# Performance work log

Hardware: AMD Instinct MI355X
Metric: run time of the kernel (lower is better)

Reference implementation:

```python
import jax, jax.numpy as jnp
import numpy as np

INF = 1e20


def setup_inputs() -> dict:
    key = jax.random.key(0)
    k1, k2, k3 = jax.random.split(key, 3)
    B, Q, M, F, D = 16, 64, 512, 16, 512
    return {
        "query_embed": jax.random.normal(k1, (B, Q, D), dtype=jnp.float32),
        "in_memory_embed": jax.random.normal(k2, (B, M, F, D), dtype=jnp.float32),
        "out_memory_embed": jax.random.normal(k3, (B, M, F, D), dtype=jnp.float32),
        "ctx_mask": jnp.ones((B, M, F), dtype=jnp.float32),
        "query_mask": jnp.ones((B, Q), dtype=jnp.float32),
    }


def reference(query_embed, in_memory_embed, out_memory_embed, ctx_mask, query_mask):
    # co-attention scores: [B, Q, M, F]
    attention = jnp.einsum("bqd,bmfd->bqmf", query_embed, in_memory_embed)
    # additive INF masking (torch: mask*att - (1-mask)*INF)
    cm = ctx_mask[:, None, :, :]            # [B,1,M,F]
    attention = cm * attention - (1.0 - cm) * INF
    qm = query_mask[:, :, None, None]       # [B,Q,1,1]
    attention = qm * attention - (1.0 - qm) * INF
    # NOTE: torch code computes a max-pool over Q for kb_feature_att but
    # immediately overwrites it with softmax of a ones/ctx mask -> dead code.
    mask = ctx_mask * 1.0 - (1.0 - ctx_mask) * INF        # [B,M,F]
    kb_feature_att = jax.nn.softmax(mask, axis=-1)        # [B,M,F]
    # weighted read over feature slots: [B,M,D]
    in_mem = jnp.einsum("bmf,bmfd->bmd", kb_feature_att, in_memory_embed)
    out_mem = out_memory_embed.sum(axis=2)                # [B,M,D]
    # max-pool over feature axis F -> [B,Q,M]
    att_qm = attention.max(axis=-1)
    probs = jax.nn.softmax(att_qm, axis=-1)               # over M
    new_query_embed = query_embed + jnp.einsum("bqm,bmd->bqd", probs, out_mem)
    probs2 = jax.nn.softmax(att_qm, axis=1)               # over Q
    in_mem = in_mem + jnp.einsum("bqm,bqd->bmd", probs2, new_query_embed)
    return (new_query_embed, in_mem, out_mem)
```

## Files before the change

kernel.cpp:

```cpp
#include <hip/hip_runtime.h>

#define INF_F 1e20f
#define B_ 16
#define Q_ 64
#define M_ 512
#define F_ 16
#define D_ 512

typedef __attribute__((ext_vector_type(8))) short short8v;
typedef __attribute__((ext_vector_type(4))) float f32x4;

static __device__ __forceinline__ float bits_f(unsigned int u) { return __uint_as_float(u); }

static __device__ __forceinline__ int lds_off(int row, int gran) {
    return row * 40 + ((gran ^ (row & 3)) << 3);
}

static __device__ __forceinline__ void split4(float4 v, uint2& H, uint2& L) {
    unsigned hx = __float_as_uint(v.x) & 0xffff0000u, hy = __float_as_uint(v.y) & 0xffff0000u;
    unsigned hz = __float_as_uint(v.z) & 0xffff0000u, hw = __float_as_uint(v.w) & 0xffff0000u;
    H.x = (hx >> 16) | hy;
    H.y = (hz >> 16) | hw;
    L.x = (__float_as_uint(v.x - bits_f(hx)) >> 16) | (__float_as_uint(v.y - bits_f(hy)) & 0xffff0000u);
    L.y = (__float_as_uint(v.z - bits_f(hz)) >> 16) | (__float_as_uint(v.w - bits_f(hw)) & 0xffff0000u);
}

static __device__ __forceinline__ void conv_store(short* __restrict__ Hb, short* __restrict__ Lb,
                                                  int row, int c, float4 v) {
    uint2 H, L;
    split4(v, H, L);
    int off = row * 40 + (((c >> 1) ^ (row & 3)) << 3) + ((c & 1) << 2);
    *(uint2*)&Hb[off] = H;
    *(uint2*)&Lb[off] = L;
}

__global__ __launch_bounds__(256) void k_q_split(
    const float* __restrict__ q, uint2* __restrict__ qh, uint2* __restrict__ ql)
{
    int fid = blockIdx.x * 256 + threadIdx.x;
    float4 v = ((const float4*)q)[fid];
    int col = fid & 127, row = (fid >> 7) & 63, b = fid >> 13;
    int kc = col >> 3, sub = col & 7;
    uint2 H, L;
    split4(v, H, L);
    size_t oidx = ((size_t)(b * 16 + kc) * 512) + row * 8 + sub;
    qh[oidx] = H;
    ql[oidx] = L;
}

__global__ __launch_bounds__(256) void k_att_mfma(
    const uint2* __restrict__ qhg, const uint2* __restrict__ qlg,
    const float* __restrict__ in_mem, const float* __restrict__ out_mem,
    const float* __restrict__ ctx_mask, const float* __restrict__ query_mask,
    float* __restrict__ att_qm, float* __restrict__ in_mem_base,
    float* __restrict__ out_mem_sum)
{
    __shared__ __align__(16) short Qh[2][2560];
    __shared__ __align__(16) short Ql[2][2560];
    __shared__ __align__(16) short Mh[2][2560];
    __shared__ __align__(16) short Ml[2][2560];

    const int bid = blockIdx.x;
    const int b   = bid & 15;
    const int m0  = (bid >> 4) * 4;
    const int t   = threadIdx.x;
    const int w   = t >> 6;
    const int lane = t & 63;
    const int lr  = lane & 15;
    const int lg  = lane >> 4;
    const int r0  = (t >> 3) * 2, r1 = r0 + 1;
    const int scol = t & 7;
    const int f0  = r0 & 15, f1 = f0 + 1;

    float w0, w1;
    {
        const float* cm = ctx_mask + ((size_t)b * M_ + m0 + w) * F_;
        float wv[F_]; float mx = -INF_F;
        #pragma unroll
        for (int f = 0; f < F_; ++f) {
            float cv = cm[f];
            float v = cv - (1.0f - cv) * INF_F;
            wv[f] = v; mx = fmaxf(mx, v);
        }
        float s = 0.f;
        #pragma unroll
        for (int f = 0; f < F_; ++f) { wv[f] = __expf(wv[f] - mx); s += wv[f]; }
        float inv = 1.0f / s;
        w0 = wv[f0] * inv; w1 = wv[f1] * inv;
    }

    const float4* m4 = (const float4*)in_mem;
    const float4* o4 = (const float4*)out_mem;
    const size_t mbase = ((size_t)b * M_ + m0) * F_ * 128;
    const size_t qimg  = (size_t)b * 16 * 512;

    f32x4 acc[4];
    #pragma unroll
    for (int j = 0; j < 4; ++j) acc[j] = (f32x4){0, 0, 0, 0};

    uint2 qhA[2], qlA[2], qhB[2], qlB[2];
    float4 mA[2], oA[2], mB[2], oB[2];

#define LOAD_CHUNK(qh_, ql_, m_, o_, kc) do { int k4 = (kc) * 8;               \
        qh_[0] = qhg[qimg + (size_t)(kc) * 512 + t];                           \
        qh_[1] = qhg[qimg + (size_t)(kc) * 512 + t + 256];                     \
        ql_[0] = qlg[qimg + (size_t)(kc) * 512 + t];                           \
        ql_[1] = qlg[qimg + (size_t)(kc) * 512 + t + 256];                     \
        m_[0] = m4[mbase + (size_t)r0 * 128 + k4 + scol];                      \
        m_[1] = m4[mbase + (size_t)r1 * 128 + k4 + scol];                      \
        o_[0] = o4[mbase + (size_t)r0 * 128 + k4 + scol];                      \
        o_[1] = o4[mbase + (size_t)r1 * 128 + k4 + scol]; } while (0)

#define CONV(qh_, ql_, m_, bi) do {                                            \
        _Pragma("unroll")                                                      \
        for (int i = 0; i < 2; ++i) {                                          \
            int idx = t + i * 256, row = idx >> 3, sub = idx & 7;              \
            int off = row * 40 + (((sub >> 1) ^ (row & 3)) << 3) + ((sub & 1) << 2); \
            *(uint2*)&Qh[bi][off] = qh_[i];                                    \
            *(uint2*)&Ql[bi][off] = ql_[i];                                    \
        }                                                                      \
        conv_store(Mh[bi], Ml[bi], r0, scol, m_[0]);                           \
        conv_store(Mh[bi], Ml[bi], r1, scol, m_[1]); } while (0)

#define BARRIER() do { asm volatile("s_waitcnt lgkmcnt(0)" ::: "memory");      \
        __builtin_amdgcn_s_barrier(); } while (0)

#define MFMA_RED(bi, m_, o_, kc) do {                                          \
        short8v bh = *(const short8v*)&Mh[bi][lds_off(w * 16 + lr, lg)];       \
        short8v bl = *(const short8v*)&Ml[bi][lds_off(w * 16 + lr, lg)];       \
        _Pragma("unroll")                                                      \
        for (int tq = 0; tq < 4; ++tq) {                                       \
            short8v ah = *(const short8v*)&Qh[bi][lds_off(tq * 16 + lr, lg)];  \
            short8v al = *(const short8v*)&Ql[bi][lds_off(tq * 16 + lr, lg)];  \
            acc[tq] = __builtin_amdgcn_mfma_f32_16x16x32_bf16(ah, bh, acc[tq], 0, 0, 0); \
            acc[tq] = __builtin_amdgcn_mfma_f32_16x16x32_bf16(ah, bl, acc[tq], 0, 0, 0); \
            acc[tq] = __builtin_amdgcn_mfma_f32_16x16x32_bf16(al, bh, acc[tq], 0, 0, 0); \
        }                                                                      \
        float4 pin, pout;                                                      \
        pin.x = w0 * m_[0].x + w1 * m_[1].x;  pin.y = w0 * m_[0].y + w1 * m_[1].y; \
        pin.z = w0 * m_[0].z + w1 * m_[1].z;  pin.w = w0 * m_[0].w + w1 * m_[1].w; \
        pout.x = o_[0].x + o_[1].x;  pout.y = o_[0].y + o_[1].y;               \
        pout.z = o_[0].z + o_[1].z;  pout.w = o_[0].w + o_[1].w;               \
        _Pragma("unroll")                                                      \
        for (int sh = 8; sh <= 32; sh <<= 1) {                                 \
            pin.x += __shfl_xor(pin.x, sh, 64);  pin.y += __shfl_xor(pin.y, sh, 64);  \
            pin.z += __shfl_xor(pin.z, sh, 64);  pin.w += __shfl_xor(pin.w, sh, 64);  \
            pout.x += __shfl_xor(pout.x, sh, 64); pout.y += __shfl_xor(pout.y, sh, 64); \
            pout.z += __shfl_xor(pout.z, sh, 64); pout.w += __shfl_xor(pout.w, sh, 64); \
        }                                                                      \
        if (lane < 8) {                                                        \
            size_t oi = ((size_t)b * M_ + m0 + w) * 128 + (kc) * 8 + lane;     \
            ((float4*)in_mem_base)[oi] = pin;                                  \
            ((float4*)out_mem_sum)[oi] = pout;                                 \
        } } while (0)

    LOAD_CHUNK(qhA, qlA, mA, oA, 0);
    #pragma unroll
    for (int it = 0; it < 8; ++it) {
        int kc0 = 2 * it, kc1 = 2 * it + 1;
        LOAD_CHUNK(qhB, qlB, mB, oB, kc1);
        CONV(qhA, qlA, mA, 0);
        BARRIER();
        MFMA_RED(0, mA, oA, kc0);
        if (it < 7) LOAD_CHUNK(qhA, qlA, mA, oA, kc0 + 2);
        CONV(qhB, qlB, mB, 1);
        BARRIER();
        MFMA_RED(1, mB, oB, kc1);
    }

    {
        int m = m0 + w;
        float cmv = ctx_mask[((size_t)b * M_ + m) * F_ + lr];
        #pragma unroll
        for (int tq = 0; tq < 4; ++tq) {
            #pragma unroll
            for (int rg = 0; rg < 4; ++rg) {
                int q = tq * 16 + lg * 4 + rg;
                float qmv = query_mask[b * Q_ + q];
                float v = acc[tq][rg];
                v = cmv * v - (1.0f - cmv) * INF_F;
                v = qmv * v - (1.0f - qmv) * INF_F;
                #pragma unroll
                for (int sh = 1; sh < 16; sh <<= 1) v = fmaxf(v, __shfl_xor(v, sh, 64));
                if (lr == 0)
                    att_qm[((size_t)b * Q_ + q) * M_ + m] = v;
            }
        }
    }
#undef LOAD_CHUNK
#undef CONV
#undef BARRIER
#undef MFMA_RED
}

__global__ __launch_bounds__(128) void k_new_query(
    const float* __restrict__ att, const float* __restrict__ query,
    const float* __restrict__ out_sum, float* __restrict__ new_q)
{
    __shared__ float P[8][512];
    int bid = blockIdx.x;
    int b = bid & 15, qc = bid >> 4;
    int t = threadIdx.x;
    {
        int qi = t >> 4, l16 = t & 15;
        const float* row = att + ((size_t)b * Q_ + qc * 8 + qi) * M_;
        float vals[32]; float mx = -INF_F;
        #pragma unroll
        for (int i = 0; i < 32; ++i) { vals[i] = row[l16 + i * 16]; mx = fmaxf(mx, vals[i]); }
        #pragma unroll
        for (int s = 1; s < 16; s <<= 1) mx = fmaxf(mx, __shfl_xor(mx, s, 64));
        float sm = 0.f;
        #pragma unroll
        for (int i = 0; i < 32; ++i) { vals[i] = __expf(vals[i] - mx); sm += vals[i]; }
        #pragma unroll
        for (int s = 1; s < 16; s <<= 1) sm += __shfl_xor(sm, s, 64);
        float inv = 1.0f / sm;
        #pragma unroll
        for (int i = 0; i < 32; ++i) P[qi][l16 + i * 16] = vals[i] * inv;
    }
    __syncthreads();
    int c = t;
    const float4* o4 = (const float4*)out_sum + (size_t)b * M_ * 128 + c;
    const float4* q4 = (const float4*)query + ((size_t)b * Q_ + qc * 8) * 128 + c;
    float4 acc[8];
    #pragma unroll
    for (int qi = 0; qi < 8; ++qi) acc[qi] = q4[(size_t)qi * 128];
    for (int mm = 0; mm < M_; mm += 4) {
        float4 o0 = o4[(size_t)(mm + 0) * 128];
        float4 o1 = o4[(size_t)(mm + 1) * 128];
        float4 o2 = o4[(size_t)(mm + 2) * 128];
        float4 o3 = o4[(size_t)(mm + 3) * 128];
        #pragma unroll
        for (int qi = 0; qi < 8; ++qi) {
            float4 p = *(const float4*)&P[qi][mm];
            acc[qi].x += p.x * o0.x + p.y * o1.x + p.z * o2.x + p.w * o3.x;
            acc[qi].y += p.x * o0.y + p.y * o1.y + p.z * o2.y + p.w * o3.y;
            acc[qi].z += p.x * o0.z + p.y * o1.z + p.z * o2.z + p.w * o3.z;
            acc[qi].w += p.x * o0.w + p.y * o1.w + p.z * o2.w + p.w * o3.w;
        }
    }
    float4* n4 = (float4*)new_q + ((size_t)b * Q_ + qc * 8) * 128 + c;
    #pragma unroll
    for (int qi = 0; qi < 8; ++qi) n4[(size_t)qi * 128] = acc[qi];
}

__global__ __launch_bounds__(128) void k_in_mem(
    const float* __restrict__ att, const float* __restrict__ new_q,
    float* __restrict__ in_mem_io)
{
    __shared__ float P[8][64];
    int bid = blockIdx.x;
    int b = bid & 15, mc = bid >> 4;
    int m0 = mc * 8;
    int t = threadIdx.x;
    {
        int mi = t >> 4, l16 = t & 15;
        float v[4]; float mx = -INF_F;
        #pragma unroll
        for (int i = 0; i < 4; ++i) {
            v[i] = att[((size_t)b * Q_ + l16 + i * 16) * M_ + m0 + mi];
            mx = fmaxf(mx, v[i]);
        }
        #pragma unroll
        for (int s = 1; s < 16; s <<= 1) mx = fmaxf(mx, __shfl_xor(mx, s, 64));
        float sm = 0.f;
        #pragma unroll
        for (int i = 0; i < 4; ++i) { v[i] = __expf(v[i] - mx); sm += v[i]; }
        #pragma unroll
        for (int s = 1; s < 16; s <<= 1) sm += __shfl_xor(sm, s, 64);
        float inv = 1.0f / sm;
        #pragma unroll
        for (int i = 0; i < 4; ++i) P[mi][l16 + i * 16] = v[i] * inv;
    }
    __syncthreads();
    int c = t;
    float4* io = (float4*)in_mem_io + ((size_t)b * M_ + m0) * 128 + c;
    const float4* n4 = (const float4*)new_q + (size_t)b * Q_ * 128 + c;
    float4 acc[8];
    #pragma unroll
    for (int mi = 0; mi < 8; ++mi) acc[mi] = io[(size_t)mi * 128];
    for (int q = 0; q < Q_; q += 4) {
        float4 n0 = n4[(size_t)(q + 0) * 128];
        float4 n1 = n4[(size_t)(q + 1) * 128];
        float4 n2 = n4[(size_t)(q + 2) * 128];
        float4 n3 = n4[(size_t)(q + 3) * 128];
        #pragma unroll
        for (int mi = 0; mi < 8; ++mi) {
            float4 p = *(const float4*)&P[mi][q];
            acc[mi].x += p.x * n0.x + p.y * n1.x + p.z * n2.x + p.w * n3.x;
            acc[mi].y += p.x * n0.y + p.y * n1.y + p.z * n2.y + p.w * n3.y;
            acc[mi].z += p.x * n0.z + p.y * n1.z + p.z * n2.z + p.w * n3.z;
            acc[mi].w += p.x * n0.w + p.y * n1.w + p.z * n2.w + p.w * n3.w;
        }
    }
    #pragma unroll
    for (int mi = 0; mi < 8; ++mi) io[(size_t)mi * 128] = acc[mi];
}

extern "C" void kernel_launch(void* const* d_in, const int* in_sizes, int n_in,
                              void* d_out, int out_size, void* d_ws, size_t ws_size,
                              hipStream_t stream)
{
    const float* query      = (const float*)d_in[0];
    const float* in_mem     = (const float*)d_in[1];
    const float* out_mem    = (const float*)d_in[2];
    const float* ctx_mask   = (const float*)d_in[3];
    const float* query_mask = (const float*)d_in[4];

    float* out = (float*)d_out;
    float* new_q      = out;
    float* in_mem_out = out + (size_t)B_*Q_*D_;
    float* out_mem_o  = in_mem_out + (size_t)B_*M_*D_;

    float* ws     = (float*)d_ws;
    float* att_qm = ws;
    uint2* qh     = (uint2*)(ws + (size_t)B_*Q_*M_);
    uint2* ql     = qh + (size_t)B_*16*512;

    hipLaunchKernelGGL(k_q_split, dim3(B_*Q_*128/256), dim3(256), 0, stream,
                       query, qh, ql);
    hipLaunchKernelGGL(k_att_mfma, dim3((M_/4) * B_), dim3(256), 0, stream,
                       qh, ql, in_mem, out_mem, ctx_mask, query_mask,
                       att_qm, in_mem_out, out_mem_o);
    hipLaunchKernelGGL(k_new_query, dim3(8 * B_), dim3(128), 0, stream,
                       att_qm, query, out_mem_o, new_q);
    hipLaunchKernelGGL(k_in_mem, dim3(64 * B_), dim3(128), 0, stream,
                       att_qm, new_q, in_mem_out);
}
```

Baseline: 238.0 us.

## Load Q fragments directly to registers and double M tile per block

k_q_split now writes Q hi/lo bf16 split data in MFMA fragment order, so the attention kernel loads A operands straight into registers instead of staging Q through LDS. Each block now covers 8 memory rows (128 M-rows per k-chunk), so every wave computes two MFMA row tiles and reuses its Q fragments across them. The feature-sum reductions for in_mem and out_mem are split between the two halves of the block with per-thread weighted sums, replacing the shuffle-tree reduction. In exchange, the grid has half as many blocks and each thread holds more registers, which may lower occupancy.

```diff
diff --git a/kernel.cpp b/kernel.cpp
--- a/kernel.cpp
+++ b/kernel.cpp
@@ -10,11 +10,7 @@
 typedef __attribute__((ext_vector_type(8))) short short8v;
 typedef __attribute__((ext_vector_type(4))) float f32x4;
 
-static __device__ __forceinline__ float bits_f(unsigned int u) { return __uint_as_float(u); }
-
-static __device__ __forceinline__ int lds_off(int row, int gran) {
-    return row * 40 + ((gran ^ (row & 3)) << 3);
-}
+static __device__ __forceinline__ float bits_f(unsigned u) { return __uint_as_float(u); }
 
 static __device__ __forceinline__ void split4(float4 v, uint2& H, uint2& L) {
     unsigned hx = __float_as_uint(v.x) & 0xffff0000u, hy = __float_as_uint(v.y) & 0xffff0000u;
@@ -25,151 +21,158 @@
     L.y = (__float_as_uint(v.z - bits_f(hz)) >> 16) | (__float_as_uint(v.w - bits_f(hw)) & 0xffff0000u);
 }
 
-static __device__ __forceinline__ void conv_store(short* __restrict__ Hb, short* __restrict__ Lb,
-                                                  int row, int c, float4 v) {
-    uint2 H, L;
-    split4(v, H, L);
-    int off = row * 40 + (((c >> 1) ^ (row & 3)) << 3) + ((c & 1) << 2);
-    *(uint2*)&Hb[off] = H;
-    *(uint2*)&Lb[off] = L;
-}
-
 __global__ __launch_bounds__(256) void k_q_split(
-    const float* __restrict__ q, uint2* __restrict__ qh, uint2* __restrict__ ql)
-{
-    int fid = blockIdx.x * 256 + threadIdx.x;
-    float4 v = ((const float4*)q)[fid];
-    int col = fid & 127, row = (fid >> 7) & 63, b = fid >> 13;
-    int kc = col >> 3, sub = col & 7;
-    uint2 H, L;
-    split4(v, H, L);
-    size_t oidx = ((size_t)(b * 16 + kc) * 512) + row * 8 + sub;
-    qh[oidx] = H;
-    ql[oidx] = L;
+    const float* __restrict__ q, short8v* __restrict__ qh, short8v* __restrict__ ql)
+{
+    int u = blockIdx.x * 256 + threadIdx.x;
+    int row = u & 63, lg = (u >> 6) & 3, kc = (u >> 8) & 15, b = u >> 12;
+    const float4* q4 = (const float4*)q;
+    size_t s = (size_t)(b * 64 + row) * 128 + kc * 8 + lg * 2;
+    float4 v0 = q4[s], v1 = q4[s + 1];
+    uint2 H0, L0, H1, L1;
+    split4(v0, H0, L0);
+    split4(v1, H1, L1);
+    uint4 H = make_uint4(H0.x, H0.y, H1.x, H1.y);
+    uint4 L = make_uint4(L0.x, L0.y, L1.x, L1.y);
+    *(uint4*)&qh[u] = H;
+    *(uint4*)&ql[u] = L;
 }
 
 __global__ __launch_bounds__(256) void k_att_mfma(
-    const uint2* __restrict__ qhg, const uint2* __restrict__ qlg,
+    const short8v* __restrict__ qh, const short8v* __restrict__ ql,
     const float* __restrict__ in_mem, const float* __restrict__ out_mem,
     const float* __restrict__ ctx_mask, const float* __restrict__ query_mask,
     float* __restrict__ att_qm, float* __restrict__ in_mem_base,
     float* __restrict__ out_mem_sum)
 {
-    __shared__ __align__(16) short Qh[2][2560];
-    __shared__ __align__(16) short Ql[2][2560];
-    __shared__ __align__(16) short Mh[2][2560];
-    __shared__ __align__(16) short Ml[2][2560];
+    __shared__ __align__(16) short Mh[2][5120];
+    __shared__ __align__(16) short Ml[2][5120];
 
     const int bid = blockIdx.x;
     const int b   = bid & 15;
-    const int m0  = (bid >> 4) * 4;
+    const int m0  = (bid >> 4) * 8;
     const int t   = threadIdx.x;
     const int w   = t >> 6;
     const int lane = t & 63;
     const int lr  = lane & 15;
     const int lg  = lane >> 4;
-    const int r0  = (t >> 3) * 2, r1 = r0 + 1;
-    const int scol = t & 7;
-    const int f0  = r0 & 15, f1 = f0 + 1;
-
-    float w0, w1;
-    {
-        const float* cm = ctx_mask + ((size_t)b * M_ + m0 + w) * F_;
-        float wv[F_]; float mx = -INF_F;
-        #pragma unroll
-        for (int f = 0; f < F_; ++f) {
-            float cv = cm[f];
-            float v = cv - (1.0f - cv) * INF_F;
+    const int r0  = t >> 3, c0 = t & 7;
+
+    const int tt   = t & 127;
+    const int msel = tt >> 4, col4 = (tt >> 1) & 7, half = tt & 1;
+    const bool is_in = (t < 128);
+
+    float wj[8];
+    if (is_in) {
+        const float* cm = ctx_mask + ((size_t)b * M_ + m0 + msel) * F_;
+        float wv[16]; float mx = -INF_F;
+        #pragma unroll
+        for (int f = 0; f < 16; ++f) {
+            float c = cm[f];
+            float v = c - (1.0f - c) * INF_F;
             wv[f] = v; mx = fmaxf(mx, v);
         }
-        float s = 0.f;
-        #pragma unroll
-        for (int f = 0; f < F_; ++f) { wv[f] = __expf(wv[f] - mx); s += wv[f]; }
-        float inv = 1.0f / s;
-        w0 = wv[f0] * inv; w1 = wv[f1] * inv;
-    }
-
-    const float4* m4 = (const float4*)in_mem;
-    const float4* o4 = (const float4*)out_mem;
-    const size_t mbase = ((size_t)b * M_ + m0) * F_ * 128;
-    const size_t qimg  = (size_t)b * 16 * 512;
-
-    f32x4 acc[4];
-    #pragma unroll
-    for (int j = 0; j < 4; ++j) acc[j] = (f32x4){0, 0, 0, 0};
-
-    uint2 qhA[2], qlA[2], qhB[2], qlB[2];
-    float4 mA[2], oA[2], mB[2], oB[2];
-
-#define LOAD_CHUNK(qh_, ql_, m_, o_, kc) do { int k4 = (kc) * 8;               \
-        qh_[0] = qhg[qimg + (size_t)(kc) * 512 + t];                           \
-        qh_[1] = qhg[qimg + (size_t)(kc) * 512 + t + 256];                     \
-        ql_[0] = qlg[qimg + (size_t)(kc) * 512 + t];                           \
-        ql_[1] = qlg[qimg + (size_t)(kc) * 512 + t + 256];                     \
-        m_[0] = m4[mbase + (size_t)r0 * 128 + k4 + scol];                      \
-        m_[1] = m4[mbase + (size_t)r1 * 128 + k4 + scol];                      \
-        o_[0] = o4[mbase + (size_t)r0 * 128 + k4 + scol];                      \
-        o_[1] = o4[mbase + (size_t)r1 * 128 + k4 + scol]; } while (0)
-
-#define CONV(qh_, ql_, m_, bi) do {                                            \
-        _Pragma("unroll")                                                      \
-        for (int i = 0; i < 2; ++i) {                                          \
-            int idx = t + i * 256, row = idx >> 3, sub = idx & 7;              \
-            int off = row * 40 + (((sub >> 1) ^ (row & 3)) << 3) + ((sub & 1) << 2); \
-            *(uint2*)&Qh[bi][off] = qh_[i];                                    \
-            *(uint2*)&Ql[bi][off] = ql_[i];                                    \
-        }                                                                      \
-        conv_store(Mh[bi], Ml[bi], r0, scol, m_[0]);                           \
-        conv_store(Mh[bi], Ml[bi], r1, scol, m_[1]); } while (0)
-
-#define BARRIER() do { asm volatile("s_waitcnt lgkmcnt(0)" ::: "memory");      \
-        __builtin_amdgcn_s_barrier(); } while (0)
-
-#define MFMA_RED(bi, m_, o_, kc) do {                                          \
-        short8v bh = *(const short8v*)&Mh[bi][lds_off(w * 16 + lr, lg)];       \
-        short8v bl = *(const short8v*)&Ml[bi][lds_off(w * 16 + lr, lg)];       \
-        _Pragma("unroll")                                                      \
-        for (int tq = 0; tq < 4; ++tq) {                                       \
-            short8v ah = *(const short8v*)&Qh[bi][lds_off(tq * 16 + lr, lg)];  \
-            short8v al = *(const short8v*)&Ql[bi][lds_off(tq * 16 + lr, lg)];  \
-            acc[tq] = __builtin_amdgcn_mfma_f32_16x16x32_bf16(ah, bh, acc[tq], 0, 0, 0); \
-            acc[tq] = __builtin_amdgcn_mfma_f32_16x16x32_bf16(ah, bl, acc[tq], 0, 0, 0); \
-            acc[tq] = __builtin_amdgcn_mfma_f32_16x16x32_bf16(al, bh, acc[tq], 0, 0, 0); \
-        }                                                                      \
-        float4 pin, pout;                                                      \
-        pin.x = w0 * m_[0].x + w1 * m_[1].x;  pin.y = w0 * m_[0].y + w1 * m_[1].y; \
-        pin.z = w0 * m_[0].z + w1 * m_[1].z;  pin.w = w0 * m_[0].w + w1 * m_[1].w; \
-        pout.x = o_[0].x + o_[1].x;  pout.y = o_[0].y + o_[1].y;               \
-        pout.z = o_[0].z + o_[1].z;  pout.w = o_[0].w + o_[1].w;               \
-        _Pragma("unroll")                                                      \
-        for (int sh = 8; sh <= 32; sh <<= 1) {                                 \
-            pin.x += __shfl_xor(pin.x, sh, 64);  pin.y += __shfl_xor(pin.y, sh, 64);  \
-            pin.z += __shfl_xor(pin.z, sh, 64);  pin.w += __shfl_xor(pin.w, sh, 64);  \
-            pout.x += __shfl_xor(pout.x, sh, 64); pout.y += __shfl_xor(pout.y, sh, 64); \
-            pout.z += __shfl_xor(pout.z, sh, 64); pout.w += __shfl_xor(pout.w, sh, 64); \
-        }                                                                      \
-        if (lane < 8) {                                                        \
-            size_t oi = ((size_t)b * M_ + m0 + w) * 128 + (kc) * 8 + lane;     \
-            ((float4*)in_mem_base)[oi] = pin;                                  \
-            ((float4*)out_mem_sum)[oi] = pout;                                 \
-        } } while (0)
-
-    LOAD_CHUNK(qhA, qlA, mA, oA, 0);
-    #pragma unroll
+        float sum = 0.f;
+        #pragma unroll
+        for (int f = 0; f < 16; ++f) { wv[f] = __expf(wv[f] - mx); sum += wv[f]; }
+        float inv = 1.0f / sum;
+        #pragma unroll
+        for (int j = 0; j < 8; ++j) wj[j] = wv[half * 8 + j] * inv;
+    } else {
+        #pragma unroll
+        for (int j = 0; j < 8; ++j) wj[j] = 1.0f;
+    }
+
+    const float4* in4 = (const float4*)in_mem;
+    const float4* ot4 = (const float4*)out_mem;
+    const size_t mb    = (size_t)((b * M_ + m0) * F_) * 128;
+    const float4* fsrc = is_in ? in4 : ot4;
+    float4* fdst       = is_in ? (float4*)in_mem_base : (float4*)out_mem_sum;
+    const size_t fbase = (size_t)((b * M_ + m0 + msel) * F_ + half * 8) * 128 + col4;
+    const size_t fob   = (size_t)(b * M_ + m0 + msel) * 128 + col4;
+    const int qbase0   = b * 16 * 256 + lg * 64 + lr;
+
+    f32x4 acc[2][4];
+    #pragma unroll
+    for (int i = 0; i < 2; ++i)
+        #pragma unroll
+        for (int j = 0; j < 4; ++j) acc[i][j] = (f32x4){0, 0, 0, 0};
+
+    float4 stg[4], fv[8];
+    short8v qfh[4], qfl[4];
+
+    #pragma unroll
+    for (int i = 0; i < 4; ++i) stg[i] = in4[mb + (size_t)(r0 + i * 32) * 128 + c0];
+    #pragma unroll
+    for (int j = 0; j < 8; ++j) fv[j] = fsrc[fbase + (size_t)j * 128];
+    #pragma unroll
+    for (int tq = 0; tq < 4; ++tq) { qfh[tq] = qh[qbase0 + tq * 16]; qfl[tq] = ql[qbase0 + tq * 16]; }
+
+#define BODY(kc_, bi_) do {                                                      \
+                                              \
+        _Pragma("unroll")                                                        \
+        for (int i = 0; i < 4; ++i) {                                            \
+            int r = r0 + i * 32;                                                 \
+            uint2 H, L; split4(stg[i], H, L);                                    \
+            int off = r * 40 + (((c0 >> 1) ^ ((r & 1) << 1)) << 3) + ((c0 & 1) << 2); \
+            *(uint2*)&Mh[bi_][off] = H;                                          \
+            *(uint2*)&Ml[bi_][off] = L;                                          \
+        }                                                                        \
+        if ((kc_) < 15) {                                                        \
+            _Pragma("unroll")                                                    \
+            for (int i = 0; i < 4; ++i)                                          \
+                stg[i] = in4[mb + (size_t)(r0 + i * 32) * 128 + ((kc_) + 1) * 8 + c0]; \
+        }                                                                        \
+        asm volatile("s_waitcnt lgkmcnt(0)" ::: "memory");                       \
+        __builtin_amdgcn_s_barrier();                                            \
+                                                 \
+        _Pragma("unroll")                                                        \
+        for (int tm = 0; tm < 2; ++tm) {                                         \
+            int row = (2 * w + tm) * 16 + lr;                                    \
+            int off = row * 40 + ((lg ^ ((row & 1) << 1)) << 3);                 \
+            short8v bh = *(const short8v*)&Mh[bi_][off];                         \
+            short8v bl = *(const short8v*)&Ml[bi_][off];                         \
+            _Pragma("unroll")                                                    \
+            for (int tq = 0; tq < 4; ++tq) {                                     \
+                acc[tm][tq] = __builtin_amdgcn_mfma_f32_16x16x32_bf16(qfh[tq], bh, acc[tm][tq], 0, 0, 0); \
+                acc[tm][tq] = __builtin_amdgcn_mfma_f32_16x16x32_bf16(qfh[tq], bl, acc[tm][tq], 0, 0, 0); \
+                acc[tm][tq] = __builtin_amdgcn_mfma_f32_16x16x32_bf16(qfl[tq], bh, acc[tm][tq], 0, 0, 0); \
+            }                                                                    \
+        }                                                                        \
+        if ((kc_) < 15) {                                                        \
+            int qb = qbase0 + ((kc_) + 1) * 256;                                 \
+            _Pragma("unroll")                                                    \
+            for (int tq = 0; tq < 4; ++tq) { qfh[tq] = qh[qb + tq * 16]; qfl[tq] = ql[qb + tq * 16]; } \
+        }                                                                        \
+                                                           \
+        {                                                                        \
+            float4 s = make_float4(0, 0, 0, 0);                                  \
+            _Pragma("unroll")                                                    \
+            for (int j = 0; j < 8; ++j) {                                        \
+                s.x += wj[j] * fv[j].x; s.y += wj[j] * fv[j].y;                  \
+                s.z += wj[j] * fv[j].z; s.w += wj[j] * fv[j].w;                  \
+            }                                                                    \
+            if ((kc_) < 15) {                                                    \
+                _Pragma("unroll")                                                \
+                for (int j = 0; j < 8; ++j)                                      \
+                    fv[j] = fsrc[fbase + (size_t)j * 128 + ((kc_) + 1) * 8];     \
+            }                                                                    \
+            s.x += __shfl_xor(s.x, 1, 64); s.y += __shfl_xor(s.y, 1, 64);        \
+            s.z += __shfl_xor(s.z, 1, 64); s.w += __shfl_xor(s.w, 1, 64);        \
+            if (half == 0) fdst[fob + (kc_) * 8] = s;                            \
+        }                                                                        \
+    } while (0)
+
     for (int it = 0; it < 8; ++it) {
         int kc0 = 2 * it, kc1 = 2 * it + 1;
-        LOAD_CHUNK(qhB, qlB, mB, oB, kc1);
-        CONV(qhA, qlA, mA, 0);
-        BARRIER();
-        MFMA_RED(0, mA, oA, kc0);
-        if (it < 7) LOAD_CHUNK(qhA, qlA, mA, oA, kc0 + 2);
-        CONV(qhB, qlB, mB, 1);
-        BARRIER();
-        MFMA_RED(1, mB, oB, kc1);
-    }
-
-    {
-        int m = m0 + w;
+        BODY(kc0, 0);
+        BODY(kc1, 1);
+    }
+#undef BODY
+
+    #pragma unroll
+    for (int tm = 0; tm < 2; ++tm) {
+        int m = m0 + 2 * w + tm;
         float cmv = ctx_mask[((size_t)b * M_ + m) * F_ + lr];
         #pragma unroll
         for (int tq = 0; tq < 4; ++tq) {
@@ -177,7 +180,7 @@
             for (int rg = 0; rg < 4; ++rg) {
                 int q = tq * 16 + lg * 4 + rg;
                 float qmv = query_mask[b * Q_ + q];
-                float v = acc[tq][rg];
+                float v = acc[tm][tq][rg];
                 v = cmv * v - (1.0f - cmv) * INF_F;
                 v = qmv * v - (1.0f - qmv) * INF_F;
                 #pragma unroll
@@ -187,10 +190,6 @@
             }
         }
     }
-#undef LOAD_CHUNK
-#undef CONV
-#undef BARRIER
-#undef MFMA_RED
 }
 
 __global__ __launch_bounds__(128) void k_new_query(
@@ -312,14 +311,13 @@
     float* in_mem_out = out + (size_t)B_*Q_*D_;
     float* out_mem_o  = in_mem_out + (size_t)B_*M_*D_;
 
-    float* ws     = (float*)d_ws;
-    float* att_qm = ws;
-    uint2* qh     = (uint2*)(ws + (size_t)B_*Q_*M_);
-    uint2* ql     = qh + (size_t)B_*16*512;
-
-    hipLaunchKernelGGL(k_q_split, dim3(B_*Q_*128/256), dim3(256), 0, stream,
-                       query, qh, ql);
-    hipLaunchKernelGGL(k_att_mfma, dim3((M_/4) * B_), dim3(256), 0, stream,
+    float* ws       = (float*)d_ws;
+    float* att_qm   = ws;
+    short8v* qh     = (short8v*)(ws + (size_t)B_*Q_*M_);
+    short8v* ql     = qh + 65536;
+
+    hipLaunchKernelGGL(k_q_split, dim3(256), dim3(256), 0, stream, query, qh, ql);
+    hipLaunchKernelGGL(k_att_mfma, dim3((M_/8) * B_), dim3(256), 0, stream,
                        qh, ql, in_mem, out_mem, ctx_mask, query_mask,
                        att_qm, in_mem_out, out_mem_o);
     hipLaunchKernelGGL(k_new_query, dim3(8 * B_), dim3(128), 0, stream,
```

Result: slower. 249.6 us (+4.9%).
